# Kernel tuning notes

Measured on AMD Instinct MI355X. Metric: run time of the kernel, lower is better.

## Reference

```python
import jax, jax.numpy as jnp
import numpy as np
import math

B, S, D, H = 16, 1024, 512, 8
DPH = D // H


def _lorentz_linear(x, W, b, log_scale):
    # LorentzLinear.forward: linear map then project onto hyperboloid
    x = x @ W.T + b
    time = jax.nn.sigmoid(x[..., :1]) * jnp.exp(log_scale) + 1.0 + 1e-4
    rest = x[..., 1:]
    sq = jnp.clip(jnp.sum(rest * rest, axis=-1, keepdims=True), 1e-8, None)
    scale = (time * time - 1.0) / sq
    return jnp.concatenate([time, rest * jnp.sqrt(scale)], axis=-1)


def setup_inputs() -> dict:
    key = jax.random.key(0)
    ks = jax.random.split(key, 16)
    stdv = 1.0 / math.sqrt(D)

    def mk_w(k):
        W = jax.random.uniform(k, (D, D), minval=-stdv, maxval=stdv, dtype=jnp.float32)
        return W.at[:, 0].set(0.0)  # reset_parameters zeroes column 0

    inp = {
        'key': jax.random.normal(ks[0], (B, S, D), dtype=jnp.float32),
        'value': jax.random.normal(ks[1], (B, S, D), dtype=jnp.float32),
        'query': jax.random.normal(ks[2], (B, S, D), dtype=jnp.float32),
        'Wq': mk_w(ks[3]), 'bq': jnp.zeros((D,), jnp.float32), 'lsq': jnp.asarray(math.log(10.0), jnp.float32),
        'Wk': mk_w(ks[4]), 'bk': jnp.zeros((D,), jnp.float32), 'lsk': jnp.asarray(math.log(10.0), jnp.float32),
        'Wv': mk_w(ks[5]), 'bv': jnp.zeros((D,), jnp.float32), 'lsv': jnp.asarray(math.log(10.0), jnp.float32),
        'attn_scale': jnp.asarray([math.sqrt(D)], jnp.float32),
        'attn_bias': jnp.zeros((), jnp.float32),
    }
    return inp


def reference(key, value, query, Wq, bq, lsq, Wk, bk, lsk, Wv, bv, lsv, attn_scale, attn_bias):
    q = _lorentz_linear(query, Wq, bq, lsq)  # [B,S,D]
    k = _lorentz_linear(key, Wk, bk, lsk)
    v = _lorentz_linear(value, Wv, bv, lsv)

    def shape(x):
        b, s, _ = x.shape
        return x.reshape(b, s, H, DPH).transpose(0, 2, 1, 3)  # [B,H,S,dph]

    q, k, v = shape(q), shape(k), shape(v)

    # Minkowski signature (-,+,...,+) on the per-head feature dim
    sgn = jnp.concatenate([-jnp.ones((1,), q.dtype), jnp.ones((DPH - 1,), q.dtype)])

    # attn = (2 + 2 * cinner(q, k)) / scale + bias  (no softmax, per source)
    attn = (2.0 + 2.0 * jnp.einsum('bhqd,bhkd->bhqk', q * sgn, k)) / attn_scale + attn_bias

    # mid_point: ave = attn @ v, then normalize by sqrt(|<ave,ave>_L|)
    ave = jnp.einsum('bhqk,bhkd->bhqd', attn, v)
    inner = jnp.sum(ave * ave * sgn, axis=-1, keepdims=True)  # Lorentz inner product
    denom = jnp.sqrt(jnp.clip(jnp.abs(inner), 1e-8, None))
    ctx = ave / denom  # [B,H,S,dph]

    b = ctx.shape[0]
    return ctx.transpose(0, 2, 1, 3).reshape(b, -1, H * DPH)  # [B,S,D]
```

## Files before the change

### kernel.cpp

```cpp
#include <hip/hip_runtime.h>
#include <stdint.h>

#define B_    16
#define S_    1024
#define D_    512
#define H_    8
#define DPH_  64
#define MTOT  (B_*S_)
#define STR   40

typedef __attribute__((ext_vector_type(8))) short  short8;
typedef __attribute__((ext_vector_type(4))) float  float4v;
typedef __attribute__((ext_vector_type(4))) ushort u16x4;

__device__ inline float bf2f(ushort u) {
    union { uint32_t u; float f; } c; c.u = ((uint32_t)u) << 16; return c.f;
}
__device__ inline ushort f2bf(float f) {
    union { float f; uint32_t u; } c; c.f = f;
    uint32_t x = c.u;
    return (ushort)((x + 0x7fffu + ((x >> 16) & 1u)) >> 16);
}
__device__ inline bool mode_f32(const void* as) {
    return ((const ushort*)as)[0] == (ushort)0x04F3u;
}
__device__ inline float lorentz_time(float y0, float ls) {
    return (1.f / (1.f + expf(-y0))) * expf(ls) + 1.0f + 1e-4f;
}

__global__ __launch_bounds__(256) void gemm_proj(
    const void* __restrict__ Xq, const void* __restrict__ Xk, const void* __restrict__ Xv,
    const void* __restrict__ Wq, const void* __restrict__ Wk, const void* __restrict__ Wv,
    const void* __restrict__ bq, const void* __restrict__ bk, const void* __restrict__ bv,
    const void* __restrict__ as_flag,
    float* __restrict__ Yq, float* __restrict__ Yk, float* __restrict__ Yv,
    float* __restrict__ RowY0, float* __restrict__ RowSq)
{
    const int z = blockIdx.z;
    const void* X    = z == 0 ? Xq : (z == 1 ? Xk : Xv);
    const void* W    = z == 0 ? Wq : (z == 1 ? Wk : Wv);
    const void* bias = z == 0 ? bq : (z == 1 ? bk : bv);
    float*      Y    = z == 0 ? Yq : (z == 1 ? Yk : Yv);
    const bool  f32  = mode_f32(as_flag);

    const int m0   = blockIdx.x * 128;
    const int n0   = blockIdx.y * 128;
    const int tid  = threadIdx.x;
    const int lane = tid & 63;
    const int w    = tid >> 6;
    const int wm   = w >> 1, wn = w & 1;

    __shared__ __align__(16) char smem[40960];
    ushort* s16 = (ushort*)smem;

    float4v acc[4][4];
    #pragma unroll
    for (int i = 0; i < 4; ++i)
        #pragma unroll
        for (int j = 0; j < 4; ++j)
            acc[i][j] = (float4v){0.f, 0.f, 0.f, 0.f};

    const int fr = lane & 15;
    const int fk = (lane >> 4) * 8;
    int offA[4], offB[4];
    #pragma unroll
    for (int i = 0; i < 4; ++i) offA[i] = (wm * 64 + i * 16 + fr) * STR + fk;
    #pragma unroll
    for (int j = 0; j < 4; ++j) offB[j] = (wn * 64 + j * 16 + fr) * STR + fk;

    if (!f32) {
        const ushort* Xu = (const ushort*)X;
        const ushort* Wu = (const ushort*)W;
        const int ra0 = tid >> 2;
        const int ka0 = (tid & 3) * 8;
        const ushort* pA0 = Xu + (size_t)(m0 + ra0) * D_ + ka0;
        const ushort* pA1 = Xu + (size_t)(m0 + ra0 + 64) * D_ + ka0;
        const ushort* pB0 = Wu + (size_t)(n0 + ra0) * D_ + ka0;
        const ushort* pB1 = Wu + (size_t)(n0 + ra0 + 64) * D_ + ka0;
        const int da0 = ra0 * STR + ka0;
        const int da1 = da0 + 64 * STR;

        {
            short8 a0 = *(const short8*)pA0;
            short8 a1 = *(const short8*)pA1;
            short8 b0 = *(const short8*)pB0;
            short8 b1 = *(const short8*)pB1;
            *(short8*)&s16[da0]        = a0;
            *(short8*)&s16[da1]        = a1;
            *(short8*)&s16[5120 + da0] = b0;
            *(short8*)&s16[5120 + da1] = b1;
        }
        short8 cA0 = *(const short8*)(pA0 + 32);
        short8 cA1 = *(const short8*)(pA1 + 32);
        short8 cB0 = *(const short8*)(pB0 + 32);
        short8 cB1 = *(const short8*)(pB1 + 32);
        __syncthreads();

        #pragma unroll
        for (int ti = 0; ti < 16; ++ti) {
            short8 nA0, nA1, nB0, nB1;
            if (ti + 2 < 16) {
                const int kt = (ti + 2) * 32;
                nA0 = *(const short8*)(pA0 + kt);
                nA1 = *(const short8*)(pA1 + kt);
                nB0 = *(const short8*)(pB0 + kt);
                nB1 = *(const short8*)(pB1 + kt);
            }
            const ushort* bb = &s16[(ti & 1) * 10240];
            short8 ah[4], bh4[4];
            #pragma unroll
            for (int i = 0; i < 4; ++i) ah[i] = *(const short8*)&bb[offA[i]];
            #pragma unroll
            for (int j = 0; j < 4; ++j) bh4[j] = *(const short8*)&bb[5120 + offB[j]];
            #pragma unroll
            for (int i = 0; i < 4; ++i)
                #pragma unroll
                for (int j = 0; j < 4; ++j)
                    acc[i][j] = __builtin_amdgcn_mfma_f32_16x16x32_bf16(ah[i], bh4[j], acc[i][j], 0, 0, 0);
            if (ti + 1 < 16) {
                ushort* nb = &s16[((ti + 1) & 1) * 10240];
                *(short8*)&nb[da0]        = cA0;
                *(short8*)&nb[da1]        = cA1;
                *(short8*)&nb[5120 + da0] = cB0;
                *(short8*)&nb[5120 + da1] = cB1;
            }
            __syncthreads();
            if (ti + 2 < 16) { cA0 = nA0; cA1 = nA1; cB0 = nB0; cB1 = nB1; }
        }
    } else {
        const float* Xf = (const float*)X;
        const float* Wf = (const float*)W;
        for (int kt = 0; kt < D_; kt += 32) {
            __syncthreads();
            u16x4 rbl[4];
            #pragma unroll
            for (int it = 0; it < 4; ++it) {
                const int c = tid + it * 256;
                const int row = c >> 3, c4 = (c & 7) * 4;
                const float4 fa = *(const float4*)&Xf[(size_t)(m0 + row) * D_ + kt + c4];
                const float4 fb = *(const float4*)&Wf[(size_t)(n0 + row) * D_ + kt + c4];
                u16x4 ah4, al4, bh4v;
                #pragma unroll
                for (int q = 0; q < 4; ++q) {
                    const float fav = (&fa.x)[q], fbv = (&fb.x)[q];
                    const ushort ha = f2bf(fav), hb = f2bf(fbv);
                    ah4[q] = ha; al4[q] = f2bf(fav - bf2f(ha));
                    bh4v[q] = hb; rbl[it][q] = f2bf(fbv - bf2f(hb));
                }
                *(u16x4*)&s16[row * STR + c4]         = ah4;
                *(u16x4*)&s16[5120 + row * STR + c4]  = al4;
                *(u16x4*)&s16[10240 + row * STR + c4] = bh4v;
            }
            __syncthreads();
            short8 ah[4], al[4], bx[4];
            #pragma unroll
            for (int i = 0; i < 4; ++i) {
                ah[i] = *(const short8*)&s16[offA[i]];
                al[i] = *(const short8*)&s16[5120 + offA[i]];
            }
            #pragma unroll
            for (int j = 0; j < 4; ++j) bx[j] = *(const short8*)&s16[10240 + offB[j]];
            #pragma unroll
            for (int i = 0; i < 4; ++i)
                #pragma unroll
                for (int j = 0; j < 4; ++j) {
                    acc[i][j] = __builtin_amdgcn_mfma_f32_16x16x32_bf16(ah[i], bx[j], acc[i][j], 0, 0, 0);
                    acc[i][j] = __builtin_amdgcn_mfma_f32_16x16x32_bf16(al[i], bx[j], acc[i][j], 0, 0, 0);
                }
            __syncthreads();
            #pragma unroll
            for (int it = 0; it < 4; ++it) {
                const int c = tid + it * 256;
                const int row = c >> 3, c4 = (c & 7) * 4;
                *(u16x4*)&s16[10240 + row * STR + c4] = rbl[it];
            }
            __syncthreads();
            #pragma unroll
            for (int j = 0; j < 4; ++j) bx[j] = *(const short8*)&s16[10240 + offB[j]];
            #pragma unroll
            for (int i = 0; i < 4; ++i)
                #pragma unroll
                for (int j = 0; j < 4; ++j)
                    acc[i][j] = __builtin_amdgcn_mfma_f32_16x16x32_bf16(ah[i], bx[j], acc[i][j], 0, 0, 0);
        }
    }

    __syncthreads();
    float* sRS = (float*)smem;
    const int er = lane >> 4;
    float bvf[4];
    #pragma unroll
    for (int j = 0; j < 4; ++j) {
        const int n = n0 + wn * 64 + j * 16 + fr;
        bvf[j] = f32 ? ((const float*)bias)[n] : bf2f(((const ushort*)bias)[n]);
    }
    #pragma unroll
    for (int i = 0; i < 4; ++i)
        #pragma unroll
        for (int r = 0; r < 4; ++r) {
            const int row = wm * 64 + i * 16 + er * 4 + r;
            const int m = m0 + row;
            float rsum = 0.f;
            #pragma unroll
            for (int j = 0; j < 4; ++j) {
                const int n = n0 + wn * 64 + j * 16 + fr;
                const float y = acc[i][j][r] + bvf[j];
                Y[(size_t)m * D_ + n] = y;
                if (n != 0) rsum += y * y;
            }
            rsum += __shfl_xor(rsum, 1, 64);
            rsum += __shfl_xor(rsum, 2, 64);
            rsum += __shfl_xor(rsum, 4, 64);
            rsum += __shfl_xor(rsum, 8, 64);
            if (fr == 0) sRS[wn * 128 + row] = rsum;
            if (blockIdx.y == 0 && wn == 0 && fr == 0)
                RowY0[z * MTOT + m] = acc[i][0][r] + bvf[0];
        }
    __syncthreads();
    if (tid < 128) {
        const float v = sRS[tid] + sRS[128 + tid];
        atomicAdd(&RowSq[z * MTOT + m0 + tid], v);
    }
}

__global__ __launch_bounds__(256) void kv_k(
    const float* __restrict__ Yk, const float* __restrict__ Yv,
    const float* __restrict__ RowY0, const float* __restrict__ RowSq,
    const void* __restrict__ lk, const void* __restrict__ lv,
    const void* __restrict__ as_flag,
    float* __restrict__ KV, float* __restrict__ Vs)
{
    const int bh = blockIdx.x;
    const int sp = blockIdx.y;
    const int b = bh >> 3, h = bh & 7;
    const int t = threadIdx.x;
    const int td = t & 15, te = t >> 4;
    const bool f32 = mode_f32(as_flag);

    __shared__ float sK[16][64];
    __shared__ float sV[16][64];
    __shared__ float sTA[4][128];

    const size_t mbase = (size_t)b * S_ + (size_t)sp * 128;
    if (t < 128) {
        const size_t m = mbase + t;
        const float lsK = f32 ? ((const float*)lk)[0] : bf2f(((const ushort*)lk)[0]);
        const float lsV = f32 ? ((const float*)lv)[0] : bf2f(((const ushort*)lv)[0]);
        const float tk = lorentz_time(RowY0[MTOT + m], lsK);
        const float ak = sqrtf((tk * tk - 1.f) / fmaxf(RowSq[MTOT + m], 1e-8f));
        const float tv = lorentz_time(RowY0[2 * MTOT + m], lsV);
        const float av = sqrtf((tv * tv - 1.f) / fmaxf(RowSq[2 * MTOT + m], 1e-8f));
        sTA[0][t] = tk; sTA[1][t] = ak; sTA[2][t] = tv; sTA[3][t] = av;
    }

    float acc[4][4] = {};
    float vs[4] = {0.f, 0.f, 0.f, 0.f};

    const int r  = t >> 4;
    const int c4 = (t & 15) * 4;

    for (int sc = 0; sc < 128; sc += 16) {
        const int lr = sc + r;
        const size_t m = mbase + lr;
        __syncthreads();
        float4 kr = *(const float4*)&Yk[m * D_ + h * DPH_ + c4];
        float4 vr = *(const float4*)&Yv[m * D_ + h * DPH_ + c4];
        const float ak = sTA[1][lr], tk = sTA[0][lr];
        const float av = sTA[3][lr], tv = sTA[2][lr];
        kr.x *= ak; kr.y *= ak; kr.z *= ak; kr.w *= ak;
        vr.x *= av; vr.y *= av; vr.z *= av; vr.w *= av;
        if (h == 0 && c4 == 0) { kr.x = tk; vr.x = tv; }
        *(float4*)&sK[r][c4] = kr;
        *(float4*)&sV[r][c4] = vr;
        __syncthreads();
        #pragma unroll
        for (int rr = 0; rr < 16; ++rr) {
            const float4 k4 = *(const float4*)&sK[rr][te * 4];
            const float4 v4 = *(const float4*)&sV[rr][td * 4];
            #pragma unroll
            for (int i = 0; i < 4; ++i)
                #pragma unroll
                for (int j = 0; j < 4; ++j)
                    acc[i][j] += (&k4.x)[i] * (&v4.x)[j];
            #pragma unroll
            for (int j = 0; j < 4; ++j) vs[j] += (&v4.x)[j];
        }
    }

    #pragma unroll
    for (int i = 0; i < 4; ++i)
        #pragma unroll
        for (int j = 0; j < 4; ++j)
            atomicAdd(&KV[(size_t)bh * 4096 + (te * 4 + i) * 64 + td * 4 + j],
                      acc[i][j]);
    if (te == 0) {
        #pragma unroll
        for (int j = 0; j < 4; ++j)
            atomicAdd(&Vs[(size_t)bh * 64 + td * 4 + j], vs[j]);
    }
}

__global__ __launch_bounds__(256) void ave_norm(
    const float* __restrict__ Yq,
    const float* __restrict__ RowY0, const float* __restrict__ RowSq,
    const void* __restrict__ lq,
    const float* __restrict__ KV, const float* __restrict__ Vs,
    const void* __restrict__ as_ptr, const void* __restrict__ ab_ptr,
    void* __restrict__ outp)
{
    const int bh = blockIdx.x >> 3;
    const int st = blockIdx.x & 7;
    const int b = bh >> 3, h = bh & 7;
    const int s0 = st * 128;
    const int t = threadIdx.x;
    const int lane = t & 63;
    const int w = t >> 6;
    const bool f32 = mode_f32(as_ptr);

    __shared__ ushort sKVh[64 * 64];
    __shared__ ushort sKVl[64 * 64];
    __shared__ ushort sQh[128 * 64];
    __shared__ ushort sQl[128 * 64];
    __shared__ float  sVs[64];
    __shared__ float  sTQ[2][128];

    if (t < 128) {
        const size_t m = (size_t)b * S_ + s0 + t;
        const float lsQ = f32 ? ((const float*)lq)[0] : bf2f(((const ushort*)lq)[0]);
        const float tq = lorentz_time(RowY0[m], lsQ);
        const float aq = sqrtf((tq * tq - 1.f) / fmaxf(RowSq[m], 1e-8f));
        sTQ[0][t] = tq; sTQ[1][t] = aq;
    }
    #pragma unroll
    for (int i = 0; i < 16; ++i) {
        const int idx = t + i * 256;
        const int e = idx >> 6, d = idx & 63;
        const float v = KV[(size_t)bh * 4096 + idx];
        const ushort hi = f2bf(v);
        sKVh[d * 64 + e] = hi;
        sKVl[d * 64 + e] = f2bf(v - bf2f(hi));
    }
    if (t < 64) sVs[t] = Vs[(size_t)bh * 64 + t];
    __syncthreads();
    #pragma unroll
    for (int i = 0; i < 8; ++i) {
        const int idx = t + i * 256;
        const int row = idx >> 4, c4 = (idx & 15) * 4;
        const size_t m = (size_t)b * S_ + s0 + row;
        const float4 q4 = *(const float4*)&Yq[m * D_ + h * DPH_ + c4];
        const float alpha = sTQ[1][row], tim = sTQ[0][row];
        #pragma unroll
        for (int q = 0; q < 4; ++q) {
            const int col = c4 + q;
            float val = (&q4.x)[q] * alpha;
            if (h == 0 && col == 0) val = tim;
            if (col == 0) val = -val;
            const ushort hi = f2bf(val);
            sQh[row * 64 + col] = hi;
            sQl[row * 64 + col] = f2bf(val - bf2f(hi));
        }
    }
    __syncthreads();

    const float asv = f32 ? ((const float*)as_ptr)[0] : bf2f(((const ushort*)as_ptr)[0]);
    const float abv = f32 ? ((const float*)ab_ptr)[0] : bf2f(((const ushort*)ab_ptr)[0]);
    const float c1f = 2.0f / asv;
    const float c0f = c1f + abv;

    const int fr = lane & 15, fq = lane >> 4;

    float4v acc[2][4];
    #pragma unroll
    for (int mi = 0; mi < 2; ++mi)
        #pragma unroll
        for (int j = 0; j < 4; ++j)
            acc[mi][j] = (float4v){0.f, 0.f, 0.f, 0.f};

    #pragma unroll
    for (int kk = 0; kk < 2; ++kk) {
        const int ko = kk * 32 + fq * 8;
        short8 ah[2], al[2], bh4[4], bl4[4];
        #pragma unroll
        for (int mi = 0; mi < 2; ++mi) {
            ah[mi] = *(const short8*)&sQh[(w * 32 + mi * 16 + fr) * 64 + ko];
            al[mi] = *(const short8*)&sQl[(w * 32 + mi * 16 + fr) * 64 + ko];
        }
        #pragma unroll
        for (int j = 0; j < 4; ++j) {
            bh4[j] = *(const short8*)&sKVh[(j * 16 + fr) * 64 + ko];
            bl4[j] = *(const short8*)&sKVl[(j * 16 + fr) * 64 + ko];
        }
        #pragma unroll
        for (int mi = 0; mi < 2; ++mi)
            #pragma unroll
            for (int j = 0; j < 4; ++j) {
                acc[mi][j] = __builtin_amdgcn_mfma_f32_16x16x32_bf16(ah[mi], bh4[j], acc[mi][j], 0, 0, 0);
                acc[mi][j] = __builtin_amdgcn_mfma_f32_16x16x32_bf16(ah[mi], bl4[j], acc[mi][j], 0, 0, 0);
                acc[mi][j] = __builtin_amdgcn_mfma_f32_16x16x32_bf16(al[mi], bh4[j], acc[mi][j], 0, 0, 0);
            }
    }

    #pragma unroll
    for (int mi = 0; mi < 2; ++mi) {
        float avev[4][4];
        float part[4] = {0.f, 0.f, 0.f, 0.f};
        #pragma unroll
        for (int j = 0; j < 4; ++j) {
            const float vsn = sVs[j * 16 + fr];
            #pragma unroll
            for (int r = 0; r < 4; ++r) {
                const float a = c1f * acc[mi][j][r] + c0f * vsn;
                avev[j][r] = a;
                part[r] += (j == 0 && fr == 0) ? -(a * a) : (a * a);
            }
        }
        #pragma unroll
        for (int off = 1; off < 16; off <<= 1)
            #pragma unroll
            for (int r = 0; r < 4; ++r)
                part[r] += __shfl_xor(part[r], off, 64);
        float rd[4];
        #pragma unroll
        for (int r = 0; r < 4; ++r)
            rd[r] = 1.0f / sqrtf(fmaxf(fabsf(part[r]), 1e-8f));
        #pragma unroll
        for (int j = 0; j < 4; ++j)
            #pragma unroll
            for (int r = 0; r < 4; ++r) {
                const int srow = s0 + w * 32 + mi * 16 + fq * 4 + r;
                const size_t oidx = ((size_t)b * S_ + srow) * D_ + h * DPH_ + j * 16 + fr;
                const float cv = avev[j][r] * rd[r];
                if (f32) ((float*)outp)[oidx] = cv;
                else     ((ushort*)outp)[oidx] = f2bf(cv);
            }
    }
}

extern "C" void kernel_launch(void* const* d_in, const int* in_sizes, int n_in,
                              void* d_out, int out_size, void* d_ws, size_t ws_size,
                              hipStream_t stream)
{
    const void* key    = d_in[0];
    const void* value  = d_in[1];
    const void* query  = d_in[2];
    const void* Wq     = d_in[3];
    const void* bq     = d_in[4];
    const void* lsq    = d_in[5];
    const void* Wk     = d_in[6];
    const void* bk     = d_in[7];
    const void* lsk    = d_in[8];
    const void* Wv     = d_in[9];
    const void* bv     = d_in[10];
    const void* lsv    = d_in[11];
    const void* ascale = d_in[12];
    const void* abias  = d_in[13];

    char* ws = (char*)d_ws;
    float* Yq    = (float*)(ws + 0);
    float* Yk    = (float*)(ws + 33554432);
    float* Yv    = (float*)(ws + 67108864);
    float* RowY0 = (float*)(ws + 100663296);
    float* RowSq = (float*)(ws + 100859904);
    float* KV    = (float*)(ws + 101056512);
    float* Vs    = (float*)(ws + 103153664);

    hipMemsetAsync(ws + 100859904, 0, 2326528, stream);

    gemm_proj<<<dim3(MTOT / 128, D_ / 128, 3), 256, 0, stream>>>(
        query, key, value, Wq, Wk, Wv, bq, bk, bv, ascale,
        Yq, Yk, Yv, RowY0, RowSq);
    kv_k<<<dim3(B_ * H_, 8), 256, 0, stream>>>(
        Yk, Yv, RowY0, RowSq, lsk, lsv, ascale, KV, Vs);
    ave_norm<<<B_ * H_ * (S_ / 128), 256, 0, stream>>>(
        Yq, RowY0, RowSq, lsq, KV, Vs, ascale, abias, d_out);
}
```

Before: 340.1 us.

## Use direct global-to-LDS loads with swizzle, remap GEMM grid, prefetch KV, halve ave tiles

The bf16 GEMM path now loads tiles with global_load_lds straight into an XOR-swizzled, unpadded LDS layout instead of staging through registers, with a single barrier per k-step. The 3D grid becomes a flattened 1D grid grouped so blocks that share X rows run close together, which should improve L2 reuse. kv_k prefetches the next K/V rows into registers ahead of the reduction, and ave_norm uses 64-row tiles, doubling the block count for more parallelism. The risks are a wrong swizzle or async-load ordering, and lower MFMA reuse per block in ave_norm.

```diff
diff --git a/kernel.cpp b/kernel.cpp
--- a/kernel.cpp
+++ b/kernel.cpp
@@ -7,7 +7,6 @@
 #define H_    8
 #define DPH_  64
 #define MTOT  (B_*S_)
-#define STR   40
 
 typedef __attribute__((ext_vector_type(8))) short  short8;
 typedef __attribute__((ext_vector_type(4))) float  float4v;
@@ -36,21 +35,26 @@
     float* __restrict__ Yq, float* __restrict__ Yk, float* __restrict__ Yv,
     float* __restrict__ RowY0, float* __restrict__ RowSq)
 {
-    const int z = blockIdx.z;
+    const int id    = blockIdx.x;
+    const int n_idx = (id >> 3) & 3;
+    const int zm    = (id >> 5) * 8 + (id & 7);
+    const int z     = zm >> 7;
+    const int m_idx = zm & 127;
+
     const void* X    = z == 0 ? Xq : (z == 1 ? Xk : Xv);
     const void* W    = z == 0 ? Wq : (z == 1 ? Wk : Wv);
     const void* bias = z == 0 ? bq : (z == 1 ? bk : bv);
     float*      Y    = z == 0 ? Yq : (z == 1 ? Yk : Yv);
     const bool  f32  = mode_f32(as_flag);
 
-    const int m0   = blockIdx.x * 128;
-    const int n0   = blockIdx.y * 128;
+    const int m0   = m_idx * 128;
+    const int n0   = n_idx * 128;
     const int tid  = threadIdx.x;
     const int lane = tid & 63;
     const int w    = tid >> 6;
     const int wm   = w >> 1, wn = w & 1;
 
-    __shared__ __align__(16) char smem[40960];
+    __shared__ __align__(16) char smem[32768];
     ushort* s16 = (ushort*)smem;
 
     float4v acc[4][4];
@@ -60,76 +64,79 @@
         for (int j = 0; j < 4; ++j)
             acc[i][j] = (float4v){0.f, 0.f, 0.f, 0.f};
 
-    const int fr = lane & 15;
-    const int fk = (lane >> 4) * 8;
-    int offA[4], offB[4];
-    #pragma unroll
-    for (int i = 0; i < 4; ++i) offA[i] = (wm * 64 + i * 16 + fr) * STR + fk;
-    #pragma unroll
-    for (int j = 0; j < 4; ++j) offB[j] = (wn * 64 + j * 16 + fr) * STR + fk;
+    const int fr  = lane & 15;
+    const int fk8 = lane >> 4;
 
     if (!f32) {
         const ushort* Xu = (const ushort*)X;
         const ushort* Wu = (const ushort*)W;
-        const int ra0 = tid >> 2;
-        const int ka0 = (tid & 3) * 8;
-        const ushort* pA0 = Xu + (size_t)(m0 + ra0) * D_ + ka0;
-        const ushort* pA1 = Xu + (size_t)(m0 + ra0 + 64) * D_ + ka0;
-        const ushort* pB0 = Wu + (size_t)(n0 + ra0) * D_ + ka0;
-        const ushort* pB1 = Wu + (size_t)(n0 + ra0 + 64) * D_ + ka0;
-        const int da0 = ra0 * STR + ka0;
-        const int da1 = da0 + 64 * STR;
-
-        {
-            short8 a0 = *(const short8*)pA0;
-            short8 a1 = *(const short8*)pA1;
-            short8 b0 = *(const short8*)pB0;
-            short8 b1 = *(const short8*)pB1;
-            *(short8*)&s16[da0]        = a0;
-            *(short8*)&s16[da1]        = a1;
-            *(short8*)&s16[5120 + da0] = b0;
-            *(short8*)&s16[5120 + da1] = b1;
-        }
-        short8 cA0 = *(const short8*)(pA0 + 32);
-        short8 cA1 = *(const short8*)(pA1 + 32);
-        short8 cB0 = *(const short8*)(pB0 + 32);
-        short8 cB1 = *(const short8*)(pB1 + 32);
-        __syncthreads();
-
+        const int l4 = lane >> 2;
+        const int lc = lane & 3;
+        const int rA0 = 2 * w * 16 + l4;
+        const int rA1 = rA0 + 16;
+        const int p0 = (lc ^ ((rA0 >> 1) & 3)) * 8;
+        const int p1 = (lc ^ ((rA1 >> 1) & 3)) * 8;
+        const ushort* gA0 = Xu + (size_t)(m0 + rA0) * D_ + p0;
+        const ushort* gA1 = Xu + (size_t)(m0 + rA1) * D_ + p1;
+        const ushort* gB0 = Wu + (size_t)(n0 + rA0) * D_ + p0;
+        const ushort* gB1 = Wu + (size_t)(n0 + rA1) * D_ + p1;
+        const int dA0 = 2 * w * 512;
+        const int dA1 = dA0 + 512;
+
+        int offA[4], offB[4];
+        #pragma unroll
+        for (int i = 0; i < 4; ++i) {
+            const int row = wm * 64 + i * 16 + fr;
+            offA[i] = row * 32 + ((fk8 ^ ((row >> 1) & 3)) * 8);
+        }
+        #pragma unroll
+        for (int j = 0; j < 4; ++j) {
+            const int row = wn * 64 + j * 16 + fr;
+            offB[j] = 4096 + row * 32 + ((fk8 ^ ((row >> 1) & 3)) * 8);
+        }
+
+        #define ISSUE_TILE(KT, BUFB)                                                            \
+            do {                                                                                \
+                __builtin_amdgcn_global_load_lds(                                               \
+                    (const __attribute__((address_space(1))) void*)(gA0 + (KT)),                \
+                    (__attribute__((address_space(3))) void*)&s16[(BUFB) + dA0], 16, 0, 0);     \
+                __builtin_amdgcn_global_load_lds(                                               \
+                    (const __attribute__((address_space(1))) void*)(gA1 + (KT)),                \
+                    (__attribute__((address_space(3))) void*)&s16[(BUFB) + dA1], 16, 0, 0);     \
+                __builtin_amdgcn_global_load_lds(                                               \
+                    (const __attribute__((address_space(1))) void*)(gB0 + (KT)),                \
+                    (__attribute__((address_space(3))) void*)&s16[(BUFB) + 4096 + dA0], 16, 0, 0); \
+                __builtin_amdgcn_global_load_lds(                                               \
+                    (const __attribute__((address_space(1))) void*)(gB1 + (KT)),                \
+                    (__attribute__((address_space(3))) void*)&s16[(BUFB) + 4096 + dA1], 16, 0, 0); \
+            } while (0)
+
+        ISSUE_TILE(0, 0);
         #pragma unroll
         for (int ti = 0; ti < 16; ++ti) {
-            short8 nA0, nA1, nB0, nB1;
-            if (ti + 2 < 16) {
-                const int kt = (ti + 2) * 32;
-                nA0 = *(const short8*)(pA0 + kt);
-                nA1 = *(const short8*)(pA1 + kt);
-                nB0 = *(const short8*)(pB0 + kt);
-                nB1 = *(const short8*)(pB1 + kt);
-            }
-            const ushort* bb = &s16[(ti & 1) * 10240];
+            __syncthreads();
+            if (ti + 1 < 16) ISSUE_TILE((ti + 1) * 32, ((ti + 1) & 1) * 8192);
+            const int bb = (ti & 1) * 8192;
             short8 ah[4], bh4[4];
             #pragma unroll
-            for (int i = 0; i < 4; ++i) ah[i] = *(const short8*)&bb[offA[i]];
-            #pragma unroll
-            for (int j = 0; j < 4; ++j) bh4[j] = *(const short8*)&bb[5120 + offB[j]];
+            for (int i = 0; i < 4; ++i) ah[i] = *(const short8*)&s16[bb + offA[i]];
+            #pragma unroll
+            for (int j = 0; j < 4; ++j) bh4[j] = *(const short8*)&s16[bb + offB[j]];
             #pragma unroll
             for (int i = 0; i < 4; ++i)
                 #pragma unroll
                 for (int j = 0; j < 4; ++j)
                     acc[i][j] = __builtin_amdgcn_mfma_f32_16x16x32_bf16(ah[i], bh4[j], acc[i][j], 0, 0, 0);
-            if (ti + 1 < 16) {
-                ushort* nb = &s16[((ti + 1) & 1) * 10240];
-                *(short8*)&nb[da0]        = cA0;
-                *(short8*)&nb[da1]        = cA1;
-                *(short8*)&nb[5120 + da0] = cB0;
-                *(short8*)&nb[5120 + da1] = cB1;
-            }
-            __syncthreads();
-            if (ti + 2 < 16) { cA0 = nA0; cA1 = nA1; cB0 = nB0; cB1 = nB1; }
-        }
+        }
+        #undef ISSUE_TILE
     } else {
         const float* Xf = (const float*)X;
         const float* Wf = (const float*)W;
+        int offAu[4], offBu[4];
+        #pragma unroll
+        for (int i = 0; i < 4; ++i) offAu[i] = (wm * 64 + i * 16 + fr) * 32 + fk8 * 8;
+        #pragma unroll
+        for (int j = 0; j < 4; ++j) offBu[j] = (wn * 64 + j * 16 + fr) * 32 + fk8 * 8;
         for (int kt = 0; kt < D_; kt += 32) {
             __syncthreads();
             u16x4 rbl[4];
@@ -147,19 +154,19 @@
                     ah4[q] = ha; al4[q] = f2bf(fav - bf2f(ha));
                     bh4v[q] = hb; rbl[it][q] = f2bf(fbv - bf2f(hb));
                 }
-                *(u16x4*)&s16[row * STR + c4]         = ah4;
-                *(u16x4*)&s16[5120 + row * STR + c4]  = al4;
-                *(u16x4*)&s16[10240 + row * STR + c4] = bh4v;
+                *(u16x4*)&s16[row * 32 + c4]        = ah4;
+                *(u16x4*)&s16[4096 + row * 32 + c4] = al4;
+                *(u16x4*)&s16[8192 + row * 32 + c4] = bh4v;
             }
             __syncthreads();
             short8 ah[4], al[4], bx[4];
             #pragma unroll
             for (int i = 0; i < 4; ++i) {
-                ah[i] = *(const short8*)&s16[offA[i]];
-                al[i] = *(const short8*)&s16[5120 + offA[i]];
+                ah[i] = *(const short8*)&s16[offAu[i]];
+                al[i] = *(const short8*)&s16[4096 + offAu[i]];
             }
             #pragma unroll
-            for (int j = 0; j < 4; ++j) bx[j] = *(const short8*)&s16[10240 + offB[j]];
+            for (int j = 0; j < 4; ++j) bx[j] = *(const short8*)&s16[8192 + offBu[j]];
             #pragma unroll
             for (int i = 0; i < 4; ++i)
                 #pragma unroll
@@ -172,11 +179,11 @@
             for (int it = 0; it < 4; ++it) {
                 const int c = tid + it * 256;
                 const int row = c >> 3, c4 = (c & 7) * 4;
-                *(u16x4*)&s16[10240 + row * STR + c4] = rbl[it];
+                *(u16x4*)&s16[8192 + row * 32 + c4] = rbl[it];
             }
             __syncthreads();
             #pragma unroll
-            for (int j = 0; j < 4; ++j) bx[j] = *(const short8*)&s16[10240 + offB[j]];
+            for (int j = 0; j < 4; ++j) bx[j] = *(const short8*)&s16[8192 + offBu[j]];
             #pragma unroll
             for (int i = 0; i < 4; ++i)
                 #pragma unroll
@@ -213,7 +220,7 @@
             rsum += __shfl_xor(rsum, 4, 64);
             rsum += __shfl_xor(rsum, 8, 64);
             if (fr == 0) sRS[wn * 128 + row] = rsum;
-            if (blockIdx.y == 0 && wn == 0 && fr == 0)
+            if (n_idx == 0 && wn == 0 && fr == 0)
                 RowY0[z * MTOT + m] = acc[i][0][r] + bvf[0];
         }
     __syncthreads();
@@ -259,20 +266,26 @@
     const int r  = t >> 4;
     const int c4 = (t & 15) * 4;
 
+    float4 kr = *(const float4*)&Yk[(mbase + r) * D_ + h * DPH_ + c4];
+    float4 vr = *(const float4*)&Yv[(mbase + r) * D_ + h * DPH_ + c4];
+    __syncthreads();
+
     for (int sc = 0; sc < 128; sc += 16) {
         const int lr = sc + r;
-        const size_t m = mbase + lr;
-        __syncthreads();
-        float4 kr = *(const float4*)&Yk[m * D_ + h * DPH_ + c4];
-        float4 vr = *(const float4*)&Yv[m * D_ + h * DPH_ + c4];
+        float4 k2 = kr, v2 = vr;
         const float ak = sTA[1][lr], tk = sTA[0][lr];
         const float av = sTA[3][lr], tv = sTA[2][lr];
-        kr.x *= ak; kr.y *= ak; kr.z *= ak; kr.w *= ak;
-        vr.x *= av; vr.y *= av; vr.z *= av; vr.w *= av;
-        if (h == 0 && c4 == 0) { kr.x = tk; vr.x = tv; }
-        *(float4*)&sK[r][c4] = kr;
-        *(float4*)&sV[r][c4] = vr;
+        k2.x *= ak; k2.y *= ak; k2.z *= ak; k2.w *= ak;
+        v2.x *= av; v2.y *= av; v2.z *= av; v2.w *= av;
+        if (h == 0 && c4 == 0) { k2.x = tk; v2.x = tv; }
+        *(float4*)&sK[r][c4] = k2;
+        *(float4*)&sV[r][c4] = v2;
         __syncthreads();
+        if (sc + 16 < 128) {
+            const size_t m = mbase + sc + 16 + r;
+            kr = *(const float4*)&Yk[m * D_ + h * DPH_ + c4];
+            vr = *(const float4*)&Yv[m * D_ + h * DPH_ + c4];
+        }
         #pragma unroll
         for (int rr = 0; rr < 16; ++rr) {
             const float4 k4 = *(const float4*)&sK[rr][te * 4];
@@ -285,6 +298,7 @@
             #pragma unroll
             for (int j = 0; j < 4; ++j) vs[j] += (&v4.x)[j];
         }
+        __syncthreads();
     }
 
     #pragma unroll
@@ -308,10 +322,10 @@
     const void* __restrict__ as_ptr, const void* __restrict__ ab_ptr,
     void* __restrict__ outp)
 {
-    const int bh = blockIdx.x >> 3;
-    const int st = blockIdx.x & 7;
+    const int bh = blockIdx.x >> 4;
+    const int st = blockIdx.x & 15;
     const int b = bh >> 3, h = bh & 7;
-    const int s0 = st * 128;
+    const int s0 = st * 64;
     const int t = threadIdx.x;
     const int lane = t & 63;
     const int w = t >> 6;
@@ -319,12 +333,12 @@
 
     __shared__ ushort sKVh[64 * 64];
     __shared__ ushort sKVl[64 * 64];
-    __shared__ ushort sQh[128 * 64];
-    __shared__ ushort sQl[128 * 64];
+    __shared__ ushort sQh[64 * 64];
+    __shared__ ushort sQl[64 * 64];
     __shared__ float  sVs[64];
-    __shared__ float  sTQ[2][128];
-
-    if (t < 128) {
+    __shared__ float  sTQ[2][64];
+
+    if (t < 64) {
         const size_t m = (size_t)b * S_ + s0 + t;
         const float lsQ = f32 ? ((const float*)lq)[0] : bf2f(((const ushort*)lq)[0]);
         const float tq = lorentz_time(RowY0[m], lsQ);
@@ -343,7 +357,7 @@
     if (t < 64) sVs[t] = Vs[(size_t)bh * 64 + t];
     __syncthreads();
     #pragma unroll
-    for (int i = 0; i < 8; ++i) {
+    for (int i = 0; i < 4; ++i) {
         const int idx = t + i * 256;
         const int row = idx >> 4, c4 = (idx & 15) * 4;
         const size_t m = (size_t)b * S_ + s0 + row;
@@ -369,71 +383,60 @@
 
     const int fr = lane & 15, fq = lane >> 4;
 
-    float4v acc[2][4];
-    #pragma unroll
-    for (int mi = 0; mi < 2; ++mi)
-        #pragma unroll
-        for (int j = 0; j < 4; ++j)
-            acc[mi][j] = (float4v){0.f, 0.f, 0.f, 0.f};
+    float4v acc[4];
+    #pragma unroll
+    for (int j = 0; j < 4; ++j) acc[j] = (float4v){0.f, 0.f, 0.f, 0.f};
 
     #pragma unroll
     for (int kk = 0; kk < 2; ++kk) {
         const int ko = kk * 32 + fq * 8;
-        short8 ah[2], al[2], bh4[4], bl4[4];
-        #pragma unroll
-        for (int mi = 0; mi < 2; ++mi) {
-            ah[mi] = *(const short8*)&sQh[(w * 32 + mi * 16 + fr) * 64 + ko];
-            al[mi] = *(const short8*)&sQl[(w * 32 + mi * 16 + fr) * 64 + ko];
-        }
+        short8 ah, al, bh4[4], bl4[4];
+        ah = *(const short8*)&sQh[(w * 16 + fr) * 64 + ko];
+        al = *(const short8*)&sQl[(w * 16 + fr) * 64 + ko];
         #pragma unroll
         for (int j = 0; j < 4; ++j) {
             bh4[j] = *(const short8*)&sKVh[(j * 16 + fr) * 64 + ko];
             bl4[j] = *(const short8*)&sKVl[(j * 16 + fr) * 64 + ko];
         }
         #pragma unroll
-        for (int mi = 0; mi < 2; ++mi)
-            #pragma unroll
-            for (int j = 0; j < 4; ++j) {
-                acc[mi][j] = __builtin_amdgcn_mfma_f32_16x16x32_bf16(ah[mi], bh4[j], acc[mi][j], 0, 0, 0);
-                acc[mi][j] = __builtin_amdgcn_mfma_f32_16x16x32_bf16(ah[mi], bl4[j], acc[mi][j], 0, 0, 0);
-                acc[mi][j] = __builtin_amdgcn_mfma_f32_16x16x32_bf16(al[mi], bh4[j], acc[mi][j], 0, 0, 0);
-            }
-    }
-
-    #pragma unroll
-    for (int mi = 0; mi < 2; ++mi) {
-        float avev[4][4];
-        float part[4] = {0.f, 0.f, 0.f, 0.f};
-        #pragma unroll
         for (int j = 0; j < 4; ++j) {
-            const float vsn = sVs[j * 16 + fr];
-            #pragma unroll
-            for (int r = 0; r < 4; ++r) {
-                const float a = c1f * acc[mi][j][r] + c0f * vsn;
-                avev[j][r] = a;
-                part[r] += (j == 0 && fr == 0) ? -(a * a) : (a * a);
-            }
-        }
-        #pragma unroll
-        for (int off = 1; off < 16; off <<= 1)
-            #pragma unroll
-            for (int r = 0; r < 4; ++r)
-                part[r] += __shfl_xor(part[r], off, 64);
-        float rd[4];
+            acc[j] = __builtin_amdgcn_mfma_f32_16x16x32_bf16(ah, bh4[j], acc[j], 0, 0, 0);
+            acc[j] = __builtin_amdgcn_mfma_f32_16x16x32_bf16(ah, bl4[j], acc[j], 0, 0, 0);
+            acc[j] = __builtin_amdgcn_mfma_f32_16x16x32_bf16(al, bh4[j], acc[j], 0, 0, 0);
+        }
+    }
+
+    float avev[4][4];
+    float part[4] = {0.f, 0.f, 0.f, 0.f};
+    #pragma unroll
+    for (int j = 0; j < 4; ++j) {
+        const float vsn = sVs[j * 16 + fr];
+        #pragma unroll
+        for (int r = 0; r < 4; ++r) {
+            const float a = c1f * acc[j][r] + c0f * vsn;
+            avev[j][r] = a;
+            part[r] += (j == 0 && fr == 0) ? -(a * a) : (a * a);
+        }
+    }
+    #pragma unroll
+    for (int off = 1; off < 16; off <<= 1)
         #pragma unroll
         for (int r = 0; r < 4; ++r)
-            rd[r] = 1.0f / sqrtf(fmaxf(fabsf(part[r]), 1e-8f));
-        #pragma unroll
-        for (int j = 0; j < 4; ++j)
-            #pragma unroll
-            for (int r = 0; r < 4; ++r) {
-                const int srow = s0 + w * 32 + mi * 16 + fq * 4 + r;
-                const size_t oidx = ((size_t)b * S_ + srow) * D_ + h * DPH_ + j * 16 + fr;
-                const float cv = avev[j][r] * rd[r];
-                if (f32) ((float*)outp)[oidx] = cv;
-                else     ((ushort*)outp)[oidx] = f2bf(cv);
-            }
-    }
+            part[r] += __shfl_xor(part[r], off, 64);
+    float rd[4];
+    #pragma unroll
+    for (int r = 0; r < 4; ++r)
+        rd[r] = 1.0f / sqrtf(fmaxf(fabsf(part[r]), 1e-8f));
+    #pragma unroll
+    for (int j = 0; j < 4; ++j)
+        #pragma unroll
+        for (int r = 0; r < 4; ++r) {
+            const int srow = s0 + w * 16 + fq * 4 + r;
+            const size_t oidx = ((size_t)b * S_ + srow) * D_ + h * DPH_ + j * 16 + fr;
+            const float cv = avev[j][r] * rd[r];
+            if (f32) ((float*)outp)[oidx] = cv;
+            else     ((ushort*)outp)[oidx] = f2bf(cv);
+        }
 }
 
 extern "C" void kernel_launch(void* const* d_in, const int* in_sizes, int n_in,
@@ -466,11 +469,11 @@
 
     hipMemsetAsync(ws + 100859904, 0, 2326528, stream);
 
-    gemm_proj<<<dim3(MTOT / 128, D_ / 128, 3), 256, 0, stream>>>(
+    gemm_proj<<<1536, 256, 0, stream>>>(
         query, key, value, Wq, Wk, Wv, bq, bk, bv, ascale,
         Yq, Yk, Yv, RowY0, RowSq);
     kv_k<<<dim3(B_ * H_, 8), 256, 0, stream>>>(
         Yk, Yv, RowY0, RowSq, lsk, lsv, ascale, KV, Vs);
-    ave_norm<<<B_ * H_ * (S_ / 128), 256, 0, stream>>>(
+    ave_norm<<<B_ * H_ * (S_ / 64), 256, 0, stream>>>(
         Yq, RowY0, RowSq, lsq, KV, Vs, ascale, abias, d_out);
 }
```

Result: slower. 358.4 us (+5.4%).
